# Kernel tuning notes

Measured on AMD Instinct MI355X. Metric: run time of the kernel, lower is better.

The kernel has to match this reference:

```python
import jax, jax.numpy as jnp
import numpy as np
import math

B, L, D = 4, 4096, 1024
M = 256  # num random features
EPS = 1e-06


def setup_inputs() -> dict:
    key = jax.random.key(0)
    kq, kk, kv, kp = jax.random.split(key, 4)
    Q = jax.random.normal(kq, (B, L, D), dtype=jnp.float32)
    K = jax.random.normal(kk, (B, L, D), dtype=jnp.float32)
    V = jax.random.normal(kv, (B, L, D), dtype=jnp.float32)
    # Gaussian random projection (ortho_features=False path): shape (num_features, d_model)
    projection = jax.random.normal(kp, (M, D), dtype=jnp.float32)
    return {"Q": Q, "K": K, "V": V, "projection": projection}


def reference(Q, K, V, projection):
    d_model = Q.shape[-1]
    m = projection.shape[0]
    inv_sqrt_d = 1.0 / math.sqrt(d_model)
    # random features: exp((x / sqrt(d)) @ P^T)
    rf_q = jnp.exp(jnp.einsum('bld,md->blm', Q * inv_sqrt_d, projection)) / math.sqrt(m)  # (B,L,M)
    rf_k = jnp.exp(jnp.einsum('bld,md->blm', K * inv_sqrt_d, projection))                 # (B,L,M)
    # linear attention: KV state and normalizer
    KV = jnp.einsum('blm,bld->bmd', rf_k, V)   # (B,M,D)
    Z = jnp.sum(rf_k, axis=1)                   # (B,M)
    out = jnp.einsum('blm,bmd->bld', rf_q, KV)  # (B,L,D)
    normalizer = jnp.einsum('blm,bm->bl', rf_q, Z) + EPS  # (B,L)
    return out / normalizer[..., None]
```

## Files before the change

### kernel.cpp

```cpp
#include <hip/hip_runtime.h>
#include <math.h>

#define NB 4
#define LL 4096
#define DD 1024
#define MM 256

typedef short s16x8 __attribute__((ext_vector_type(8)));
typedef short s16x4 __attribute__((ext_vector_type(4)));
typedef float fx4 __attribute__((ext_vector_type(4)));
typedef unsigned u32x2 __attribute__((ext_vector_type(2)));
typedef unsigned u32x4 __attribute__((ext_vector_type(4)));

__device__ __forceinline__ float b2f(short s) {
  union { unsigned u; float f; } v;
  v.u = ((unsigned)(unsigned short)s) << 16;
  return v.f;
}
__device__ __forceinline__ short f2b(float f) {
  union { float f; unsigned u; } v;
  v.f = f;
  unsigned r = (v.u + 0x7fffu + ((v.u >> 16) & 1u)) >> 16;
  return (short)(unsigned short)r;
}
__device__ __forceinline__ unsigned cvt2(float lo, float hi) {
  unsigned r;
  asm("v_cvt_pk_bf16_f32 %0, %1, %2" : "=v"(r) : "v"(lo), "v"(hi));
  return r;
}
__device__ __forceinline__ int swz(int row, int col) {
  return row * 64 + (col ^ ((row & 7) << 3));
}
__device__ __forceinline__ int keyf(int m) { return (m ^ (m >> 2)) & 3; }

typedef __attribute__((address_space(1))) const void* gas1_t;
typedef __attribute__((address_space(3))) void* las3_t;
#define GLL16(g, l) __builtin_amdgcn_global_load_lds((gas1_t)(const void*)(g), (las3_t)(void*)(l), 16, 0, 0)

__global__ __launch_bounds__(256) void k_cast(const float* __restrict__ in, short* __restrict__ out, int n4) {
  int i = blockIdx.x * 256 + threadIdx.x;
  if (i >= n4) return;
  float4 v = ((const float4*)in)[i];
  s16x4 s;
  s[0] = f2b(v.x); s[1] = f2b(v.y); s[2] = f2b(v.z); s[3] = f2b(v.w);
  ((s16x4*)out)[i] = s;
}

__global__ __launch_bounds__(512, 2) void k_qk(const float* __restrict__ Q, const float* __restrict__ K,
                                               const short* __restrict__ Pb,
                                               short* __restrict__ rfq, short* __restrict__ rfkT,
                                               float* __restrict__ Zz) {
  __shared__ short As[2][8192];
  __shared__ short Bs[2][16384];
  int b = blockIdx.z;
  int l0 = blockIdx.x * 64;
  int tid = threadIdx.x, lane = tid & 63, w = tid >> 6;
  int wr = w >> 2, wq = w & 3;
  int m16 = lane & 15, kg = lane >> 4;

  int arow = tid >> 2, acol = (tid & 3) * 16;
  int akey = (arow & 7) << 3;
  const float* Xr = (arow < 64 ? Q + ((size_t)b * LL + l0 + arow) * DD
                               : K + ((size_t)b * LL + l0 + arow - 64) * DD) + acol;

  fx4 acc[4][4] = {};
  float4 pa[4];

  #pragma unroll
  for (int i = 0; i < 4; ++i) pa[i] = *(const float4*)(Xr + i * 4);
  #pragma unroll
  for (int j = 0; j < 4; ++j) {
    int fl = tid + j * 512, row = fl >> 3, c8 = fl & 7;
    GLL16(Pb + (size_t)row * DD + (c8 ^ (row & 7)) * 8, &Bs[0][fl * 8]);
  }
  {
    u32x4 v0;
    v0[0] = cvt2(pa[0].x, pa[0].y); v0[1] = cvt2(pa[0].z, pa[0].w);
    v0[2] = cvt2(pa[1].x, pa[1].y); v0[3] = cvt2(pa[1].z, pa[1].w);
    *(u32x4*)&As[0][arow * 64 + (acol ^ akey)] = v0;
    v0[0] = cvt2(pa[2].x, pa[2].y); v0[1] = cvt2(pa[2].z, pa[2].w);
    v0[2] = cvt2(pa[3].x, pa[3].y); v0[3] = cvt2(pa[3].z, pa[3].w);
    *(u32x4*)&As[0][arow * 64 + ((acol + 8) ^ akey)] = v0;
  }
  __syncthreads();

  for (int t = 0; t < 16; ++t) {
    int cur = t & 1, nxt = cur ^ 1;
    if (t < 15) {
      int d1 = (t + 1) * 64;
      #pragma unroll
      for (int i = 0; i < 4; ++i) pa[i] = *(const float4*)(Xr + d1 + i * 4);
      #pragma unroll
      for (int j = 0; j < 4; ++j) {
        int fl = tid + j * 512, row = fl >> 3, c8 = fl & 7;
        GLL16(Pb + (size_t)row * DD + d1 + (c8 ^ (row & 7)) * 8, &Bs[nxt][fl * 8]);
      }
    }
    #pragma unroll
    for (int ks = 0; ks < 2; ++ks) {
      int kb = ks * 32 + kg * 8;
      s16x8 af[4], bf[4];
      #pragma unroll
      for (int mi = 0; mi < 4; ++mi) af[mi] = *(const s16x8*)&As[cur][swz(wr * 64 + mi * 16 + m16, kb)];
      #pragma unroll
      for (int ni = 0; ni < 4; ++ni) bf[ni] = *(const s16x8*)&Bs[cur][swz(wq * 64 + ni * 16 + m16, kb)];
      #pragma unroll
      for (int mi = 0; mi < 4; ++mi)
        #pragma unroll
        for (int ni = 0; ni < 4; ++ni)
          acc[mi][ni] = __builtin_amdgcn_mfma_f32_16x16x32_bf16(af[mi], bf[ni], acc[mi][ni], 0, 0, 0);
    }
    if (t < 15) {
      u32x4 v0;
      v0[0] = cvt2(pa[0].x, pa[0].y); v0[1] = cvt2(pa[0].z, pa[0].w);
      v0[2] = cvt2(pa[1].x, pa[1].y); v0[3] = cvt2(pa[1].z, pa[1].w);
      *(u32x4*)&As[nxt][arow * 64 + (acol ^ akey)] = v0;
      v0[0] = cvt2(pa[2].x, pa[2].y); v0[1] = cvt2(pa[2].z, pa[2].w);
      v0[2] = cvt2(pa[3].x, pa[3].y); v0[3] = cvt2(pa[3].z, pa[3].w);
      *(u32x4*)&As[nxt][arow * 64 + ((acol + 8) ^ akey)] = v0;
    }
    __syncthreads();
  }

  if (wr == 0) {
    #pragma unroll
    for (int mi = 0; mi < 4; ++mi)
      #pragma unroll
      for (int ni = 0; ni < 4; ++ni) {
        int r0 = mi * 16 + (kg << 2);
        int c = wq * 64 + ni * 16 + m16;
        #pragma unroll
        for (int u = 0; u < 4; ++u)
          rfq[((size_t)b * LL + l0 + r0 + u) * MM + c] = f2b(expf(acc[mi][ni][u] * 0.03125f) * 0.0625f);
      }
  } else {
    short* T = (short*)Bs;
    float zp[4] = {0.f, 0.f, 0.f, 0.f};
    #pragma unroll
    for (int mi = 0; mi < 4; ++mi)
      #pragma unroll
      for (int ni = 0; ni < 4; ++ni) {
        int l = mi * 16 + (kg << 2);
        int m = wq * 64 + ni * 16 + m16;
        int key = (m & 7) << 3;
        float e0 = expf(acc[mi][ni][0] * 0.03125f);
        float e1 = expf(acc[mi][ni][1] * 0.03125f);
        float e2 = expf(acc[mi][ni][2] * 0.03125f);
        float e3 = expf(acc[mi][ni][3] * 0.03125f);
        zp[ni] += e0 + e1 + e2 + e3;
        *(unsigned*)&T[m * 64 + (l ^ key)] = cvt2(e0, e1);
        *(unsigned*)&T[m * 64 + ((l ^ key) + 2)] = cvt2(e2, e3);
      }
    #pragma unroll
    for (int ni = 0; ni < 4; ++ni) {
      zp[ni] += __shfl_xor(zp[ni], 16);
      zp[ni] += __shfl_xor(zp[ni], 32);
    }
    if (kg == 0) {
      #pragma unroll
      for (int ni = 0; ni < 4; ++ni)
        atomicAdd(&Zz[b * MM + wq * 64 + ni * 16 + m16], zp[ni]);
    }
  }
  __syncthreads();
  if (tid >= 256) {
    int m = tid - 256, mkey = (m & 7) << 3;
    const short* T = (const short*)Bs;
    short* dst = rfkT + ((size_t)b * MM + m) * LL + l0;
    #pragma unroll
    for (int j = 0; j < 8; ++j) {
      s16x8 v = *(const s16x8*)&T[m * 64 + ((j * 8) ^ mkey)];
      *(s16x8*)(dst + j * 8) = v;
    }
  }
}

__global__ __launch_bounds__(512, 4) void k_kv(const float* __restrict__ V, const short* __restrict__ rfkT,
                                               float* __restrict__ KVp) {
  __shared__ float Vs[2][32 * 65];
  __shared__ short Ak[2][256 * 32];
  int d0 = blockIdx.x * 64, kc = blockIdx.y, b = blockIdx.z;
  int ls = kc * 512;
  int tid = threadIdx.x, lane = tid & 63, w = tid >> 6;
  int wm = w >> 1, wd = w & 1;
  int m16 = lane & 15, kg = lane >> 4;

  int vl = tid >> 4, vf = (tid & 15) * 4;
  const float* Vb = V + ((size_t)b * LL + ls + vl) * DD + d0 + vf;

  int am = tid >> 2, as = tid & 3;
  const short* AkS0 = rfkT + ((size_t)b * MM + am) * LL + ls + (as ^ keyf(am)) * 8;
  const short* AkS1 = rfkT + ((size_t)b * MM + am + 128) * LL + ls + (as ^ keyf(am + 128)) * 8;

  fx4 acc[4][2] = {};
  float4 pv;

  pv = *(const float4*)(Vb);
  GLL16(AkS0, &Ak[0][tid * 8]);
  GLL16(AkS1, &Ak[0][(tid + 512) * 8]);
  #pragma unroll
  for (int j = 0; j < 4; ++j) Vs[0][vl * 65 + vf + j] = ((const float*)&pv)[j];
  __syncthreads();

  for (int ch = 0; ch < 16; ++ch) {
    int cur = ch & 1, nxt = cur ^ 1;
    if (ch < 15) {
      int lo = (ch + 1) * 32;
      pv = *(const float4*)(Vb + (size_t)lo * DD);
      GLL16(AkS0 + lo, &Ak[nxt][tid * 8]);
      GLL16(AkS1 + lo, &Ak[nxt][(tid + 512) * 8]);
    }
    s16x8 af[4];
    #pragma unroll
    for (int mi = 0; mi < 4; ++mi) {
      int m = wm * 64 + mi * 16 + m16;
      af[mi] = *(const s16x8*)&Ak[cur][m * 32 + ((kg ^ keyf(m)) * 8)];
    }
    #pragma unroll
    for (int ni = 0; ni < 2; ++ni) {
      int d = wd * 32 + ni * 16 + m16;
      const float* vs = &Vs[cur][kg * 8 * 65 + d];
      u32x4 bw;
      bw[0] = cvt2(vs[0], vs[65]);
      bw[1] = cvt2(vs[130], vs[195]);
      bw[2] = cvt2(vs[260], vs[325]);
      bw[3] = cvt2(vs[390], vs[455]);
      s16x8 bf = *(s16x8*)&bw;
      #pragma unroll
      for (int mi = 0; mi < 4; ++mi)
        acc[mi][ni] = __builtin_amdgcn_mfma_f32_16x16x32_bf16(af[mi], bf, acc[mi][ni], 0, 0, 0);
    }
    if (ch < 15) {
      #pragma unroll
      for (int j = 0; j < 4; ++j) Vs[nxt][vl * 65 + vf + j] = ((const float*)&pv)[j];
    }
    __syncthreads();
  }

  float* dst = KVp + (((size_t)kc * NB + b) * DD + d0) * MM;
  #pragma unroll
  for (int mi = 0; mi < 4; ++mi)
    #pragma unroll
    for (int ni = 0; ni < 2; ++ni) {
      int d = wd * 32 + ni * 16 + m16;
      int m = wm * 64 + mi * 16 + (kg << 2);
      *(float4*)(dst + (size_t)d * MM + m) = *(float4*)&acc[mi][ni];
    }
}

__global__ __launch_bounds__(256) void k_red(const float* __restrict__ KVp, short* __restrict__ KVTb) {
  int i = blockIdx.x * 256 + threadIdx.x;
  const float4* p = (const float4*)KVp;
  float4 s = p[i];
  #pragma unroll
  for (int k = 1; k < 8; ++k) {
    float4 v = p[i + k * 262144];
    s.x += v.x; s.y += v.y; s.z += v.z; s.w += v.w;
  }
  u32x2 o;
  o[0] = cvt2(s.x, s.y);
  o[1] = cvt2(s.z, s.w);
  ((u32x2*)KVTb)[i] = o;
}

__global__ __launch_bounds__(512) void k_out(const short* __restrict__ rfq, const short* __restrict__ KVTb,
                                             const float* __restrict__ Zz, float* __restrict__ out) {
  __shared__ short Aq[2][8192];
  __shared__ short Bv[2][8192];
  __shared__ float zl[256];
  __shared__ float np[512];
  __shared__ float nf[128];
  int l0 = blockIdx.x * 128, d0 = blockIdx.y * 128, b = blockIdx.z;
  int tid = threadIdx.x, lane = tid & 63, w = tid >> 6;
  int wr = w >> 2, wc = w & 3;
  const short* Ab = rfq + ((size_t)b * LL + l0) * MM;
  const short* Bb = KVTb + ((size_t)b * DD + d0) * MM;
  int f1 = tid + 512;
  int ar0 = tid >> 3, ac0 = tid & 7, ar1 = f1 >> 3, ac1 = f1 & 7;
  int nrow = tid & 127, nsub = tid >> 7;
  if (tid < 256) zl[tid] = Zz[b * MM + tid];
  fx4 acc[4][2] = {};
  float na = 0.f;

  GLL16(Ab + (size_t)ar0 * MM + (ac0 ^ (ar0 & 7)) * 8, &Aq[0][tid * 8]);
  GLL16(Ab + (size_t)ar1 * MM + (ac1 ^ (ar1 & 7)) * 8, &Aq[0][f1 * 8]);
  GLL16(Bb + (size_t)ar0 * MM + (ac0 ^ (ar0 & 7)) * 8, &Bv[0][tid * 8]);
  GLL16(Bb + (size_t)ar1 * MM + (ac1 ^ (ar1 & 7)) * 8, &Bv[0][f1 * 8]);
  __syncthreads();

  for (int t = 0; t < 4; ++t) {
    int cur = t & 1, nxt = cur ^ 1;
    if (t < 3) {
      int m1 = (t + 1) * 64;
      GLL16(Ab + (size_t)ar0 * MM + m1 + (ac0 ^ (ar0 & 7)) * 8, &Aq[nxt][tid * 8]);
      GLL16(Ab + (size_t)ar1 * MM + m1 + (ac1 ^ (ar1 & 7)) * 8, &Aq[nxt][f1 * 8]);
      GLL16(Bb + (size_t)ar0 * MM + m1 + (ac0 ^ (ar0 & 7)) * 8, &Bv[nxt][tid * 8]);
      GLL16(Bb + (size_t)ar1 * MM + m1 + (ac1 ^ (ar1 & 7)) * 8, &Bv[nxt][f1 * 8]);
    }
    #pragma unroll
    for (int kk = 0; kk < 16; ++kk) {
      int k = nsub * 16 + kk;
      na += b2f(Aq[cur][nrow * 64 + (k ^ ((nrow & 7) << 3))]) * zl[t * 64 + k];
    }
    #pragma unroll
    for (int ks = 0; ks < 2; ++ks) {
      int kb = ks * 32 + (lane >> 4) * 8;
      s16x8 af[4], bf[2];
      #pragma unroll
      for (int mi = 0; mi < 4; ++mi) {
        int row = wr * 64 + mi * 16 + (lane & 15);
        af[mi] = *(const s16x8*)&Aq[cur][row * 64 + (kb ^ ((row & 7) << 3))];
      }
      #pragma unroll
      for (int ni = 0; ni < 2; ++ni) {
        int row = wc * 32 + ni * 16 + (lane & 15);
        bf[ni] = *(const s16x8*)&Bv[cur][row * 64 + (kb ^ ((row & 7) << 3))];
      }
      #pragma unroll
      for (int mi = 0; mi < 4; ++mi)
        #pragma unroll
        for (int ni = 0; ni < 2; ++ni)
          acc[mi][ni] = __builtin_amdgcn_mfma_f32_16x16x32_bf16(af[mi], bf[ni], acc[mi][ni], 0, 0, 0);
    }
    __syncthreads();
  }
  np[tid] = na;
  __syncthreads();
  if (tid < 128) nf[tid] = np[tid] + np[tid + 128] + np[tid + 256] + np[tid + 384] + 1e-6f;
  __syncthreads();
  #pragma unroll
  for (int mi = 0; mi < 4; ++mi)
    #pragma unroll
    for (int ni = 0; ni < 2; ++ni) {
      int l = wr * 64 + mi * 16 + ((lane >> 4) << 2);
      int d = d0 + wc * 32 + ni * 16 + (lane & 15);
      #pragma unroll
      for (int u = 0; u < 4; ++u)
        out[((size_t)b * LL + l0 + l + u) * DD + d] = acc[mi][ni][u] / nf[l + u];
    }
}

extern "C" void kernel_launch(void* const* d_in, const int* in_sizes, int n_in,
                              void* d_out, int out_size, void* d_ws, size_t ws_size,
                              hipStream_t stream) {
  const float* Q = (const float*)d_in[0];
  const float* K = (const float*)d_in[1];
  const float* V = (const float*)d_in[2];
  const float* P = (const float*)d_in[3];
  float* out = (float*)d_out;
  char* ws = (char*)d_ws;

  short* Pb   = (short*)(ws + 0);
  float* Zz   = (float*)(ws + 524288);
  short* KVTb = (short*)(ws + 528384);
  short* rfq  = (short*)(ws + 4722688);
  short* rfkT = (short*)(ws + 13111296);
  float* KVp  = (float*)(ws + 21499904);

  k_cast<<<256, 256, 0, stream>>>(P, Pb, 65536);
  (void)hipMemsetAsync(Zz, 0, 4096, stream);
  k_qk<<<dim3(64, 1, NB), 512, 0, stream>>>(Q, K, Pb, rfq, rfkT, Zz);
  k_kv<<<dim3(16, 8, NB), 512, 0, stream>>>(V, rfkT, KVp);
  k_red<<<1024, 256, 0, stream>>>(KVp, KVTb);
  k_out<<<dim3(32, 8, NB), 512, 0, stream>>>(rfq, KVTb, Zz, out);
}
```

Baseline: 128.2 us.

## Widen KV tile to 128 columns and stagger QK reduction start per block

The KV accumulation kernel now covers 128 V columns per block instead of 64, which halves the grid and doubles per-wave accumulators. Each rfkT tile loaded into shared memory is therefore reused across twice as many output columns. The QK kernel also rotates the starting chunk of the D-dimension loop per block, so concurrent blocks read different parts of the projection matrix and channel or cache hotspots are spread out. In exchange, KV has higher register and LDS use with the occupancy hint removed, and only 256 blocks, which may underfill the GPU.

Measured after the change: 124.8 us. 1.03x faster.

```diff
diff --git a/kernel.cpp b/kernel.cpp
--- a/kernel.cpp
+++ b/kernel.cpp
@@ -54,6 +54,7 @@
   __shared__ short Bs[2][16384];
   int b = blockIdx.z;
   int l0 = blockIdx.x * 64;
+  int phase = (blockIdx.x + blockIdx.z * 4) & 15;
   int tid = threadIdx.x, lane = tid & 63, w = tid >> 6;
   int wr = w >> 2, wq = w & 3;
   int m16 = lane & 15, kg = lane >> 4;
@@ -66,14 +67,15 @@
   fx4 acc[4][4] = {};
   float4 pa[4];
 
-  #pragma unroll
-  for (int i = 0; i < 4; ++i) pa[i] = *(const float4*)(Xr + i * 4);
-  #pragma unroll
-  for (int j = 0; j < 4; ++j) {
-    int fl = tid + j * 512, row = fl >> 3, c8 = fl & 7;
-    GLL16(Pb + (size_t)row * DD + (c8 ^ (row & 7)) * 8, &Bs[0][fl * 8]);
-  }
   {
+    int d0 = phase * 64;
+    #pragma unroll
+    for (int i = 0; i < 4; ++i) pa[i] = *(const float4*)(Xr + d0 + i * 4);
+    #pragma unroll
+    for (int j = 0; j < 4; ++j) {
+      int fl = tid + j * 512, row = fl >> 3, c8 = fl & 7;
+      GLL16(Pb + (size_t)row * DD + d0 + (c8 ^ (row & 7)) * 8, &Bs[0][fl * 8]);
+    }
     u32x4 v0;
     v0[0] = cvt2(pa[0].x, pa[0].y); v0[1] = cvt2(pa[0].z, pa[0].w);
     v0[2] = cvt2(pa[1].x, pa[1].y); v0[3] = cvt2(pa[1].z, pa[1].w);
@@ -87,7 +89,7 @@
   for (int t = 0; t < 16; ++t) {
     int cur = t & 1, nxt = cur ^ 1;
     if (t < 15) {
-      int d1 = (t + 1) * 64;
+      int d1 = (((t + 1) + phase) & 15) * 64;
       #pragma unroll
       for (int i = 0; i < 4; ++i) pa[i] = *(const float4*)(Xr + d1 + i * 4);
       #pragma unroll
@@ -175,38 +177,44 @@
   }
 }
 
-__global__ __launch_bounds__(512, 4) void k_kv(const float* __restrict__ V, const short* __restrict__ rfkT,
-                                               float* __restrict__ KVp) {
-  __shared__ float Vs[2][32 * 65];
+__global__ __launch_bounds__(512) void k_kv(const float* __restrict__ V, const short* __restrict__ rfkT,
+                                            float* __restrict__ KVp) {
+  __shared__ float Vs[2][32 * 129];
   __shared__ short Ak[2][256 * 32];
-  int d0 = blockIdx.x * 64, kc = blockIdx.y, b = blockIdx.z;
+  int d0 = blockIdx.x * 128, kc = blockIdx.y, b = blockIdx.z;
   int ls = kc * 512;
   int tid = threadIdx.x, lane = tid & 63, w = tid >> 6;
   int wm = w >> 1, wd = w & 1;
   int m16 = lane & 15, kg = lane >> 4;
 
-  int vl = tid >> 4, vf = (tid & 15) * 4;
+  int vl = tid >> 4, vf = (tid & 15) * 8;
   const float* Vb = V + ((size_t)b * LL + ls + vl) * DD + d0 + vf;
 
   int am = tid >> 2, as = tid & 3;
-  const short* AkS0 = rfkT + ((size_t)b * MM + am) * LL + ls + (as ^ keyf(am)) * 8;
-  const short* AkS1 = rfkT + ((size_t)b * MM + am + 128) * LL + ls + (as ^ keyf(am + 128)) * 8;
-
-  fx4 acc[4][2] = {};
-  float4 pv;
-
-  pv = *(const float4*)(Vb);
+  int acs = as ^ keyf(am);
+  const short* AkS0 = rfkT + ((size_t)b * MM + am) * LL + ls + acs * 8;
+  const short* AkS1 = rfkT + ((size_t)b * MM + am + 128) * LL + ls + acs * 8;
+
+  fx4 acc[4][4] = {};
+  float4 pv0, pv1;
+
+  pv0 = *(const float4*)(Vb);
+  pv1 = *(const float4*)(Vb + 4);
   GLL16(AkS0, &Ak[0][tid * 8]);
   GLL16(AkS1, &Ak[0][(tid + 512) * 8]);
   #pragma unroll
-  for (int j = 0; j < 4; ++j) Vs[0][vl * 65 + vf + j] = ((const float*)&pv)[j];
+  for (int j = 0; j < 4; ++j) {
+    Vs[0][vl * 129 + vf + j] = ((const float*)&pv0)[j];
+    Vs[0][vl * 129 + vf + 4 + j] = ((const float*)&pv1)[j];
+  }
   __syncthreads();
 
   for (int ch = 0; ch < 16; ++ch) {
     int cur = ch & 1, nxt = cur ^ 1;
     if (ch < 15) {
       int lo = (ch + 1) * 32;
-      pv = *(const float4*)(Vb + (size_t)lo * DD);
+      pv0 = *(const float4*)(Vb + (size_t)lo * DD);
+      pv1 = *(const float4*)(Vb + (size_t)lo * DD + 4);
       GLL16(AkS0 + lo, &Ak[nxt][tid * 8]);
       GLL16(AkS1 + lo, &Ak[nxt][(tid + 512) * 8]);
     }
@@ -217,14 +225,14 @@
       af[mi] = *(const s16x8*)&Ak[cur][m * 32 + ((kg ^ keyf(m)) * 8)];
     }
     #pragma unroll
-    for (int ni = 0; ni < 2; ++ni) {
-      int d = wd * 32 + ni * 16 + m16;
-      const float* vs = &Vs[cur][kg * 8 * 65 + d];
+    for (int ni = 0; ni < 4; ++ni) {
+      int d = wd * 64 + ni * 16 + m16;
+      const float* vs = &Vs[cur][kg * 8 * 129 + d];
       u32x4 bw;
-      bw[0] = cvt2(vs[0], vs[65]);
-      bw[1] = cvt2(vs[130], vs[195]);
-      bw[2] = cvt2(vs[260], vs[325]);
-      bw[3] = cvt2(vs[390], vs[455]);
+      bw[0] = cvt2(vs[0], vs[129]);
+      bw[1] = cvt2(vs[258], vs[387]);
+      bw[2] = cvt2(vs[516], vs[645]);
+      bw[3] = cvt2(vs[774], vs[903]);
       s16x8 bf = *(s16x8*)&bw;
       #pragma unroll
       for (int mi = 0; mi < 4; ++mi)
@@ -232,7 +240,10 @@
     }
     if (ch < 15) {
       #pragma unroll
-      for (int j = 0; j < 4; ++j) Vs[nxt][vl * 65 + vf + j] = ((const float*)&pv)[j];
+      for (int j = 0; j < 4; ++j) {
+        Vs[nxt][vl * 129 + vf + j] = ((const float*)&pv0)[j];
+        Vs[nxt][vl * 129 + vf + 4 + j] = ((const float*)&pv1)[j];
+      }
     }
     __syncthreads();
   }
@@ -241,8 +252,8 @@
   #pragma unroll
   for (int mi = 0; mi < 4; ++mi)
     #pragma unroll
-    for (int ni = 0; ni < 2; ++ni) {
-      int d = wd * 32 + ni * 16 + m16;
+    for (int ni = 0; ni < 4; ++ni) {
+      int d = wd * 64 + ni * 16 + m16;
       int m = wm * 64 + mi * 16 + (kg << 2);
       *(float4*)(dst + (size_t)d * MM + m) = *(float4*)&acc[mi][ni];
     }
@@ -360,7 +371,7 @@
   k_cast<<<256, 256, 0, stream>>>(P, Pb, 65536);
   (void)hipMemsetAsync(Zz, 0, 4096, stream);
   k_qk<<<dim3(64, 1, NB), 512, 0, stream>>>(Q, K, Pb, rfq, rfkT, Zz);
-  k_kv<<<dim3(16, 8, NB), 512, 0, stream>>>(V, rfkT, KVp);
+  k_kv<<<dim3(8, 8, NB), 512, 0, stream>>>(V, rfkT, KVp);
   k_red<<<1024, 256, 0, stream>>>(KVp, KVTb);
   k_out<<<dim3(32, 8, NB), 512, 0, stream>>>(rfq, KVTb, Zz, out);
 }
```
